# Kernel tuning notes

Hardware: AMD Instinct MI355X
Metric: run time of the kernel (lower is better)

## Reference

```python
import jax, jax.numpy as jnp
import numpy as np

EPS = 1e-12  # torch F.normalize eps


def _l2norm(x):
    # F.normalize(x, dim=-1): x / max(||x||, eps)
    n = jnp.sqrt(jnp.sum(x * x, axis=-1, keepdims=True))
    return x / jnp.maximum(n, EPS)


def _similarity(h, bank):
    # h: [B, D], bank: [C, M, D] -> [B, C, M] cosine similarities
    C, M, D = bank.shape
    bank_n = _l2norm(bank.reshape(C * M, D))
    h_n = _l2norm(h)
    return (h_n @ bank_n.T).reshape(-1, C, M)


def _sim_loss(S, label, censor):
    # Vectorized translation of the per-sample Python loop in get_sim_loss.
    # S: [B, C, M]; label,censor: [B] ints.
    B, C, M = S.shape
    cm = jnp.mean(S, axis=-1)                 # per-class mean of prototype sims [B, C]
    idx = jnp.arange(C)[None, :]              # [1, C]
    lab = label[:, None]                      # [B, 1]
    onehot = idx == lab                       # row == label
    # censor == 0 (event): positive = class `label` row, negative = mean over other C-1 rows
    pos_evt = jnp.sum(jnp.where(onehot, cm, 0.0), axis=-1)
    neg_evt = jnp.sum(jnp.where(onehot, 0.0, cm), axis=-1) / (C - 1)
    # censored, label == 0: positive = mean over all rows, negative = 0
    pos_all = jnp.mean(cm, axis=-1)
    # censored, label > 0: positive = rows label..C-1, negative = rows 0..label-1
    ge = idx >= lab
    n_ge = jnp.sum(ge, axis=-1).astype(cm.dtype)        # C - label
    n_lt = jnp.maximum(lab[:, 0], 1).astype(cm.dtype)   # label (guard /0)
    pos_cen = jnp.sum(jnp.where(ge, cm, 0.0), axis=-1) / n_ge
    neg_cen = jnp.sum(jnp.where(ge, 0.0, cm), axis=-1) / n_lt
    is_evt = censor == 0
    is_l0 = (~is_evt) & (label == 0)
    pos = jnp.where(is_evt, pos_evt, jnp.where(is_l0, pos_all, pos_cen))
    neg = jnp.where(is_evt, neg_evt, jnp.where(is_l0, 0.0, neg_cen))
    return -jnp.sum(pos) + jnp.sum(neg)


def setup_inputs() -> dict:
    key = jax.random.key(0)
    k = jax.random.split(key, 6)
    B, C, M, D = 16384, 4, 512, 256
    return {
        "h_path": jax.random.normal(k[0], (B, D), dtype=jnp.float32),
        "h_geno": jax.random.normal(k[1], (B, D), dtype=jnp.float32),
        "path_prototype_bank": jax.random.normal(k[2], (C, M, D), dtype=jnp.float32),
        "geno_prototype_bank": jax.random.normal(k[3], (C, M, D), dtype=jnp.float32),
        "label": jax.random.randint(k[4], (B,), 0, C, dtype=jnp.int64 if jax.config.jax_enable_x64 else jnp.int32),
        "censor": jax.random.randint(k[5], (B,), 0, 2, dtype=jnp.int64 if jax.config.jax_enable_x64 else jnp.int32),
    }


def reference(h_path, h_geno, path_prototype_bank, geno_prototype_bank, label, censor):
    # ProSurv training-path prototype matching (input_modality='path_and_geno'):
    # path_sim_loss + geno_sim_loss, each via cosine similarity to the class
    # prototype bank followed by the censor/label masked mean reduction.
    path_sim = _similarity(h_path, path_prototype_bank)   # [B, C, M]
    geno_sim = _similarity(h_geno, geno_prototype_bank)   # [B, C, M]
    sim_loss = _sim_loss(path_sim, label, censor) + _sim_loss(geno_sim, label, censor)
    return sim_loss
```

## Files before the change

### kernel.cpp

```cpp
#include <hip/hip_runtime.h>


constexpr int NC = 4;
constexpr int NM = 512;
constexpr int ND = 256;
constexpr float EPSF = 1e-12f;

constexpr int ABLK = 64;
constexpr int ROWS_PER_ABLK  = 2 * NC * NM / ABLK;
constexpr int ROWS_PER_AWAVE = ROWS_PER_ABLK / 4;
constexpr int PART_PER_COMBO = ABLK / (2 * NC);

constexpr int BBLK = 512;
constexpr int SPB  = 32;
constexpr int CHW  = 36;
constexpr int SROW = 8 * CHW;

__device__ __forceinline__ float wave_reduce(float v) {
#pragma unroll
    for (int off = 32; off >= 1; off >>= 1)
        v += __shfl_xor(v, off, 64);
    return v;
}

__global__ __launch_bounds__(256) void bank_kernel(
    const float* __restrict__ pbank, const float* __restrict__ gbank,
    float* __restrict__ partials, float* __restrict__ bankbar,
    unsigned int* __restrict__ counterA)
{
    const int blk  = blockIdx.x;
    const int wave = threadIdx.x >> 6;
    const int lane = threadIdx.x & 63;

    float4 acc = {0.f, 0.f, 0.f, 0.f};
    const int r0 = blk * ROWS_PER_ABLK + wave * ROWS_PER_AWAVE;
#pragma unroll
    for (int rr = 0; rr < ROWS_PER_AWAVE; ++rr) {
        const int r      = r0 + rr;
        const int bank   = r >> 11;
        const int within = r & (NC * NM - 1);
        const float* src = (bank ? gbank : pbank) + (size_t)within * ND;
        const float4 v = reinterpret_cast<const float4*>(src)[lane];
        float ss = v.x * v.x + v.y * v.y + v.z * v.z + v.w * v.w;
        ss = wave_reduce(ss);
        const float inv = 1.0f / (fmaxf(sqrtf(ss), EPSF) * (float)NM);
        acc.x += v.x * inv; acc.y += v.y * inv;
        acc.z += v.z * inv; acc.w += v.w * inv;
    }

    __shared__ float4 red[4][64];
    red[wave][lane] = acc;
    __syncthreads();
    if (wave == 0) {
        float4 a = red[0][lane], b = red[1][lane];
        float4 c = red[2][lane], d = red[3][lane];
        a.x += b.x + c.x + d.x; a.y += b.y + c.y + d.y;
        a.z += b.z + c.z + d.z; a.w += b.w + c.w + d.w;
        reinterpret_cast<float4*>(partials + (size_t)blk * ND)[lane] = a;
    }
    __syncthreads();

    __shared__ bool last;
    if (threadIdx.x == 0) {
        __threadfence();
        const unsigned int old = atomicAdd(counterA, 1u);
        last = ((old & (ABLK - 1)) == ABLK - 1);
    }
    __syncthreads();

    if (last) {
        __threadfence();
        const int c = threadIdx.x >> 5;
        const int j = threadIdx.x & 31;
#pragma unroll
        for (int k = 0; k < 2; ++k) {
            const int f4 = j + k * 32;
            float4 s = {0.f, 0.f, 0.f, 0.f};
#pragma unroll
            for (int p = 0; p < PART_PER_COMBO; ++p) {
                const float4 v = reinterpret_cast<const float4*>(
                    partials + (size_t)(c * PART_PER_COMBO + p) * ND)[f4];
                s.x += v.x; s.y += v.y; s.z += v.z; s.w += v.w;
            }
            reinterpret_cast<float4*>(bankbar + (size_t)c * ND)[f4] = s;
        }
    }
}

__global__ __launch_bounds__(256) void loss_kernel(
    const float* __restrict__ hp, const float* __restrict__ hg,
    const int* __restrict__ label, const int* __restrict__ censor,
    const float* __restrict__ bankbar, float* __restrict__ lpart)
{
    __shared__ __align__(16) float hbuf[SPB * SROW];
    __shared__ __align__(16) float bb[8 * SROW];

    const int t = threadIdx.x;
    const int s = t >> 3;
    const int k = t & 7;
    const int sg = blockIdx.x * SPB + s;

#pragma unroll
    for (int it = 0; it < 2; ++it) {
        const int f4    = t + it * 256;
        const int combo = f4 >> 6;
        const int rem   = f4 & 63;
        const float4 v  = reinterpret_cast<const float4*>(bankbar)[f4];
        *reinterpret_cast<float4*>(&bb[combo * SROW + (rem >> 3) * CHW + (rem & 7) * 4]) = v;
    }

    const int l   = label[sg];
    const bool evt = (censor[sg] == 0);

    float s0[2], sc[2][NC];

#pragma unroll
    for (int md = 0; md < 2; ++md) {
        const float* src = (md ? hg : hp) + (size_t)blockIdx.x * SPB * ND;
        __syncthreads();
#pragma unroll
        for (int it = 0; it < 8; ++it) {
            const int f4  = t + it * 256;
            const int ss  = f4 >> 6;
            const int rem = f4 & 63;
            const float4 v = reinterpret_cast<const float4*>(src)[f4];
            *reinterpret_cast<float4*>(&hbuf[ss * SROW + (rem >> 3) * CHW + (rem & 7) * 4]) = v;
        }
        __syncthreads();

        const float* hrow = &hbuf[s * SROW + k * CHW];
        float4 hx[8];
#pragma unroll
        for (int j = 0; j < 8; ++j)
            hx[j] = reinterpret_cast<const float4*>(hrow)[j];

        float a0 = 0.f;
#pragma unroll
        for (int j = 0; j < 8; ++j)
            a0 += hx[j].x * hx[j].x + hx[j].y * hx[j].y
                + hx[j].z * hx[j].z + hx[j].w * hx[j].w;

        float ac[NC];
#pragma unroll
        for (int c = 0; c < NC; ++c) {
            const float* brow = &bb[(md * NC + c) * SROW + k * CHW];
            float acc = 0.f;
#pragma unroll
            for (int j = 0; j < 8; ++j) {
                const float4 w = reinterpret_cast<const float4*>(brow)[j];
                acc += hx[j].x * w.x + hx[j].y * w.y
                     + hx[j].z * w.z + hx[j].w * w.w;
            }
            ac[c] = acc;
        }

#pragma unroll
        for (int off = 1; off <= 4; off <<= 1) {
            a0 += __shfl_xor(a0, off, 64);
#pragma unroll
            for (int c = 0; c < NC; ++c)
                ac[c] += __shfl_xor(ac[c], off, 64);
        }
        s0[md] = a0;
#pragma unroll
        for (int c = 0; c < NC; ++c) sc[md][c] = ac[c];
    }

    float contrib = 0.0f;
#pragma unroll
    for (int md = 0; md < 2; ++md) {
        const float inv = 1.0f / fmaxf(sqrtf(s0[md]), EPSF);
        float sum = 0.f, cml = 0.f, sge = 0.f, slt = 0.f;
#pragma unroll
        for (int c = 0; c < NC; ++c) {
            const float x = sc[md][c] * inv;
            sum += x;
            if (c == l) cml = x;
            if (c >= l) sge += x; else slt += x;
        }
        float pos, neg;
        if (evt) {
            pos = cml;
            neg = (sum - cml) * (1.0f / (NC - 1));
        } else {
            pos = sge / (float)(NC - l);
            neg = slt / (float)(l > 0 ? l : 1);
        }
        contrib += neg - pos;
    }
    if (k != 0) contrib = 0.0f;

    contrib = wave_reduce(contrib);
    __shared__ float wpart[4];
    if ((t & 63) == 0) wpart[t >> 6] = contrib;
    __syncthreads();
    if (t == 0)
        lpart[blockIdx.x] = wpart[0] + wpart[1] + wpart[2] + wpart[3];
}

__global__ __launch_bounds__(256) void final_kernel(
    const float* __restrict__ lpart, float* __restrict__ out)
{
    const int t = threadIdx.x;
    float v = lpart[t] + lpart[t + 256];
    v = wave_reduce(v);
    __shared__ float wp[4];
    if ((t & 63) == 0) wp[t >> 6] = v;
    __syncthreads();
    if (t == 0) out[0] = wp[0] + wp[1] + wp[2] + wp[3];
}

extern "C" void kernel_launch(void* const* d_in, const int* in_sizes, int n_in,
                              void* d_out, int out_size, void* d_ws, size_t ws_size,
                              hipStream_t stream)
{
    const float* hp     = (const float*)d_in[0];
    const float* hg     = (const float*)d_in[1];
    const float* pb     = (const float*)d_in[2];
    const float* gb     = (const float*)d_in[3];
    const int*   label  = (const int*)d_in[4];
    const int*   censor = (const int*)d_in[5];
    float*       out    = (float*)d_out;

    unsigned int* counterA = (unsigned int*)d_ws;
    float* partials = (float*)((char*)d_ws + 256);
    float* bankbar  = partials + (size_t)ABLK * ND;
    float* lpart    = bankbar + 2 * NC * ND;

    bank_kernel <<<ABLK, 256, 0, stream>>>(pb, gb, partials, bankbar, counterA);
    loss_kernel <<<BBLK, 256, 0, stream>>>(hp, hg, label, censor, bankbar, lpart);
    final_kernel<<<1,    256, 0, stream>>>(lpart, out);
}
```

Before: 20.93 us.

## Load activations directly into registers and drop LDS staging in loss kernel

The loss kernel no longer stages h rows and the bank means through padded shared memory with block barriers. Each thread now loads its 32-float slice of both h_path and h_geno straight from global memory into registers up front, and reads bankbar directly from global/cache. Both modalities' shuffle reductions are merged into one pass. This removes LDS traffic and the __syncthreads between the two modalities and lets both loads be in flight together. The cost is less coalesced per-thread strided loads (each thread reads 128 contiguous bytes) and more register pressure.

```diff
diff --git a/kernel.cpp b/kernel.cpp
--- a/kernel.cpp
+++ b/kernel.cpp
@@ -13,8 +13,6 @@
 
 constexpr int BBLK = 512;
 constexpr int SPB  = 32;
-constexpr int CHW  = 36;
-constexpr int SROW = 8 * CHW;
 
 __device__ __forceinline__ float wave_reduce(float v) {
 #pragma unroll
@@ -92,78 +90,58 @@
     const int* __restrict__ label, const int* __restrict__ censor,
     const float* __restrict__ bankbar, float* __restrict__ lpart)
 {
-    __shared__ __align__(16) float hbuf[SPB * SROW];
-    __shared__ __align__(16) float bb[8 * SROW];
-
-    const int t = threadIdx.x;
-    const int s = t >> 3;
-    const int k = t & 7;
+    const int t  = threadIdx.x;
+    const int s  = t >> 3;
+    const int k  = t & 7;
     const int sg = blockIdx.x * SPB + s;
 
-#pragma unroll
-    for (int it = 0; it < 2; ++it) {
-        const int f4    = t + it * 256;
-        const int combo = f4 >> 6;
-        const int rem   = f4 & 63;
-        const float4 v  = reinterpret_cast<const float4*>(bankbar)[f4];
-        *reinterpret_cast<float4*>(&bb[combo * SROW + (rem >> 3) * CHW + (rem & 7) * 4]) = v;
-    }
-
-    const int l   = label[sg];
+    const int  l   = label[sg];
     const bool evt = (censor[sg] == 0);
 
+    const float4* hp4 = reinterpret_cast<const float4*>(hp + (size_t)sg * ND + k * 32);
+    const float4* hg4 = reinterpret_cast<const float4*>(hg + (size_t)sg * ND + k * 32);
+    float4 hx0[8], hx1[8];
+#pragma unroll
+    for (int j = 0; j < 8; ++j) hx0[j] = hp4[j];
+#pragma unroll
+    for (int j = 0; j < 8; ++j) hx1[j] = hg4[j];
+
     float s0[2], sc[2][NC];
-
 #pragma unroll
     for (int md = 0; md < 2; ++md) {
-        const float* src = (md ? hg : hp) + (size_t)blockIdx.x * SPB * ND;
-        __syncthreads();
-#pragma unroll
-        for (int it = 0; it < 8; ++it) {
-            const int f4  = t + it * 256;
-            const int ss  = f4 >> 6;
-            const int rem = f4 & 63;
-            const float4 v = reinterpret_cast<const float4*>(src)[f4];
-            *reinterpret_cast<float4*>(&hbuf[ss * SROW + (rem >> 3) * CHW + (rem & 7) * 4]) = v;
-        }
-        __syncthreads();
-
-        const float* hrow = &hbuf[s * SROW + k * CHW];
-        float4 hx[8];
-#pragma unroll
-        for (int j = 0; j < 8; ++j)
-            hx[j] = reinterpret_cast<const float4*>(hrow)[j];
+        const float4* hx = md ? hx1 : hx0;
 
         float a0 = 0.f;
 #pragma unroll
         for (int j = 0; j < 8; ++j)
             a0 += hx[j].x * hx[j].x + hx[j].y * hx[j].y
                 + hx[j].z * hx[j].z + hx[j].w * hx[j].w;
-
-        float ac[NC];
+        s0[md] = a0;
+
 #pragma unroll
         for (int c = 0; c < NC; ++c) {
-            const float* brow = &bb[(md * NC + c) * SROW + k * CHW];
+            const float4* bc = reinterpret_cast<const float4*>(
+                bankbar + (size_t)(md * NC + c) * ND + k * 32);
             float acc = 0.f;
 #pragma unroll
             for (int j = 0; j < 8; ++j) {
-                const float4 w = reinterpret_cast<const float4*>(brow)[j];
+                const float4 w = bc[j];
                 acc += hx[j].x * w.x + hx[j].y * w.y
                      + hx[j].z * w.z + hx[j].w * w.w;
             }
-            ac[c] = acc;
-        }
-
-#pragma unroll
-        for (int off = 1; off <= 4; off <<= 1) {
-            a0 += __shfl_xor(a0, off, 64);
-#pragma unroll
-            for (int c = 0; c < NC; ++c)
-                ac[c] += __shfl_xor(ac[c], off, 64);
-        }
-        s0[md] = a0;
-#pragma unroll
-        for (int c = 0; c < NC; ++c) sc[md][c] = ac[c];
+            sc[md][c] = acc;
+        }
+    }
+
+#pragma unroll
+    for (int off = 1; off <= 4; off <<= 1) {
+        s0[0] += __shfl_xor(s0[0], off, 64);
+        s0[1] += __shfl_xor(s0[1], off, 64);
+#pragma unroll
+        for (int c = 0; c < NC; ++c) {
+            sc[0][c] += __shfl_xor(sc[0][c], off, 64);
+            sc[1][c] += __shfl_xor(sc[1][c], off, 64);
+        }
     }
 
     float contrib = 0.0f;
```

New measurement: 35.10 us. +67.7%, slower.
